# Kernel optimization log

Hardware: AMD Instinct MI355X
Metric: run time of the kernel (lower is better)

Reference implementation:

```python
import jax, jax.numpy as jnp
import numpy as np

B, T, N = 8, 12, 400
C0, C1, C2 = 64, 64, 128
KS, KT, H = 3, 3, 4  # Cheb order (KS+1 kernels), temporal kernel, heads
DN = ('NHWC', 'HWIO', 'NHWC')


def setup_inputs() -> dict:
    key = jax.random.key(0)
    ks = jax.random.split(key, 12)
    rn = lambda k, shp, s: jax.random.normal(k, shp, jnp.float32) * s
    inputs = jax.random.normal(ks[0], (B, T, N, C0), jnp.float32)
    supports = rn(ks[1], (KS + 1, N, N), 0.05)           # dense Cheb poly kernels
    adj_mask = (jax.random.uniform(ks[2], (N, N)) < 0.05) | jnp.eye(N, dtype=bool)
    wt1 = rn(ks[3], (KT, 1, C0, 2 * C1), 0.1)            # GLU temporal conv
    bt1 = jnp.zeros((2 * C1,), jnp.float32)
    Wf = rn(ks[4], (H, C1, C1), 0.1)                     # per-head feature proj
    a_src = rn(ks[5], (H, C1), 0.1)
    a_dst = rn(ks[6], (H, C1), 0.1)
    Wcheb = rn(ks[7], (H, KS + 1, C1, C1), 0.1)          # per-head per-hop weights
    wt2 = rn(ks[8], (KT, 1, C1, C2), 0.1)                # relu temporal conv
    bt2 = jnp.zeros((C2,), jnp.float32)
    gamma = jnp.ones((1, 1, N, C2), jnp.float32)
    beta = jnp.zeros((1, 1, N, C2), jnp.float32)
    return dict(inputs=inputs, supports=supports, adj_mask=adj_mask, wt1=wt1,
                bt1=bt1, Wf=Wf, a_src=a_src, a_dst=a_dst, Wcheb=Wcheb,
                wt2=wt2, bt2=bt2, gamma=gamma, beta=beta)


def reference(inputs, supports, adj_mask, wt1, bt1, Wf, a_src, a_dst, Wcheb,
              wt2, bt2, gamma, beta):
    # --- temporal conv 1 (GLU), c_in == c_out so residual is the raw input ---
    conv = jax.lax.conv_general_dilated(inputs, wt1, (1, 1), 'VALID',
                                        dimension_numbers=DN) + bt1
    res = inputs[:, KT - 1:]                              # [B, T-Kt+1, N, C1]
    x = (conv[..., :C1] + res) * jax.nn.sigmoid(conv[..., C1:])

    # --- spatial attention-weighted Chebyshev graph conv (batched over B*T') ---
    b, t = x.shape[0], x.shape[1]
    xf = x.reshape(b * t, N, C1)                          # [Bt, N, C1]
    f = jnp.einsum('bnc,hco->bhno', xf, Wf)               # [Bt, H, N, C1]
    e_src = jnp.einsum('bhnc,hc->bhn', f, a_src)
    e_dst = jnp.einsum('bhnc,hc->bhn', f, a_dst)
    logits = jax.nn.leaky_relu(e_src[:, :, :, None] + e_dst[:, :, None, :], 0.2)
    logits = jnp.where(adj_mask, logits, -1e9)            # mask to graph edges
    alpha = jax.nn.softmax(logits, axis=-1)               # [Bt, H, N, N]
    out = jnp.zeros((b * t, H, N, C1), xf.dtype)
    for k in range(KS + 1):                               # small fixed hop loop
        msg = jnp.einsum('bhij,bjc->bhic', alpha * supports[k], xf)
        out = out + jnp.einsum('bhic,hco->bhio', msg, Wcheb[:, k])
    gc = out.mean(axis=1).reshape(x.shape)                # head average (is_concat=False)
    x = jax.nn.relu(gc + x)                               # residual, c_in == c_out

    # --- temporal conv 2 (relu), c_in=C1 < c_out=C2 -> zero-pad residual ---
    conv2 = jax.lax.conv_general_dilated(x, wt2, (1, 1), 'VALID',
                                         dimension_numbers=DN) + bt2
    res2 = jnp.pad(x[:, KT - 1:], ((0, 0), (0, 0), (0, 0), (0, C2 - C1)))
    y = jax.nn.relu(conv2 + res2)                         # [B, T-2(Kt-1), N, C2]

    # --- per-sample-per-step norm over (node, channel), then dropout=0 (identity) ---
    mu = jnp.mean(y, axis=(2, 3), keepdims=True)
    var = jnp.var(y, axis=(2, 3), keepdims=True)
    return (y - mu) / jnp.sqrt(var + 1e-6) * gamma + beta
```

## Files before the change

### kernel.cpp

```cpp
#include <hip/hip_runtime.h>
#include <hip/hip_bf16.h>

#define NB 8
#define NT 12
#define NN 400
#define NC0 64
#define NC1 64
#define NC2 128
#define NH 4
#define NSUP 4
#define NT1 10
#define NT2 8
#define NBT 80
#define NROW 32000
#define NROW2 25600

typedef unsigned short ushort_t;
typedef ushort_t ushort8 __attribute__((ext_vector_type(8)));
typedef ushort_t ushort4v __attribute__((ext_vector_type(4)));
typedef __attribute__((ext_vector_type(8))) short bf16x8;
typedef __attribute__((ext_vector_type(4))) float f32x4;

#define WAVE_SYNC() asm volatile("s_waitcnt lgkmcnt(0)" ::: "memory")

__device__ __forceinline__ float bf2f(ushort_t u) {
    union { unsigned int i; float f; } x; x.i = ((unsigned int)u) << 16; return x.f;
}
__device__ __forceinline__ ushort_t f2bf(float f) {
    union { float f; unsigned int i; } x; x.f = f;
    unsigned int r = x.i + 0x7fff + ((x.i >> 16) & 1);
    return (ushort_t)(r >> 16);
}
__device__ __forceinline__ unsigned cvtpk_bf16(float lo, float hi) {
    unsigned r;
    asm volatile("v_cvt_pk_bf16_f32 %0, %1, %2" : "=v"(r) : "v"(lo), "v"(hi));
    return r;
}

__global__ __launch_bounds__(256) void kprep_all(
    const float* __restrict__ in,
    const float* __restrict__ wt1, const float* __restrict__ wt2, const float* __restrict__ wch,
    const float* __restrict__ Wf, const float* __restrict__ a_src, const float* __restrict__ a_dst,
    const void* __restrict__ adj, const float* __restrict__ supports,
    ushort_t* __restrict__ xbf,
    ushort_t* __restrict__ Bt1f, ushort_t* __restrict__ Bt2f, ushort_t* __restrict__ Btf,
    ushort_t* __restrict__ Bu,
    int* __restrict__ rowcnt, int* __restrict__ rowidx, float* __restrict__ supc) {
    int bid = blockIdx.x;
    if (bid < 2400) {
        int idx = bid * 256 + threadIdx.x;
        const float4* v4 = (const float4*)in;
        float4 v = v4[idx];
        ushort4v o = { f2bf(v.x), f2bf(v.y), f2bf(v.z), f2bf(v.w) };
        *(ushort4v*)(xbf + idx * 4) = o;
    } else if (bid < 2496) {
        int f = (bid - 2400) * 256 + threadIdx.x;
        int i = f & 7, lane = (f >> 3) & 63, grp = f >> 9;
        int kb = grp % 6, q = grp / 6;
        int n = q * 16 + (lane & 15);
        int k = kb * 32 + (lane >> 4) * 8 + i;
        Bt1f[f] = f2bf(wt1[k * 128 + n]);
    } else if (bid < 2592) {
        int f = (bid - 2496) * 256 + threadIdx.x;
        int i = f & 7, lane = (f >> 3) & 63, grp = f >> 9;
        int kb = grp % 6, q = grp / 6;
        int n = q * 16 + (lane & 15);
        int k = kb * 32 + (lane >> 4) * 8 + i;
        Bt2f[f] = f2bf(wt2[k * 128 + n]);
    } else if (bid < 2848) {
        int f = (bid - 2592) * 256 + threadIdx.x;
        int i = f & 7, lane = (f >> 3) & 63;
        int kb = (f >> 9) & 31, nt = f >> 14;
        int n = nt * 16 + (lane & 15);
        int k = kb * 32 + (lane >> 4) * 8 + i;
        Btf[f] = f2bf(wch[k * 64 + n]);
    } else if (bid == 2848) {
        int tid = threadIdx.x;
        int h = tid >> 6, c = tid & 63;
        const float* w = Wf + (h * 64 + c) * 64;
        float s1 = 0.f, s2 = 0.f;
        #pragma unroll 8
        for (int o = 0; o < 64; o++) {
            s1 += w[o] * a_src[h * 64 + o];
            s2 += w[o] * a_dst[h * 64 + o];
        }
        int ks = c >> 5, kq = (c & 31) >> 3, i = c & 7;
        int baseidx = ks * 512 + (kq * 16) * 8 + i;
        Bu[baseidx + (h) * 8]      = f2bf(s1);
        Bu[baseidx + (4 + h) * 8]  = f2bf(s2);
        Bu[baseidx + (8 + h) * 8]  = 0;
        Bu[baseidx + (12 + h) * 8] = 0;
    } else {
        int wid = threadIdx.x >> 6, lane = threadIdx.x & 63;
        int i = (bid - 2849) * 4 + wid;
        if (i >= NN) return;
        int f = ((const unsigned char*)adj)[401] != 0;
        const unsigned char* ab = (const unsigned char*)adj;
        const int* ai = (const int*)adj;
        int cnt = 0;
        for (int base = 0; base < NN; base += 64) {
            int j = base + lane;
            bool m = false;
            if (j < NN) m = f ? (ab[(size_t)i * NN + j] != 0) : (ai[(size_t)i * NN + j] != 0);
            unsigned long long mask = __ballot(m);
            int pre = __popcll(mask & ((1ull << lane) - 1ull));
            if (m) {
                int t = cnt + pre;
                rowidx[i * NN + t] = j;
                if (t < 64) {
                    float4 sv;
                    sv.x = supports[0 * 160000 + i * 400 + j];
                    sv.y = supports[1 * 160000 + i * 400 + j];
                    sv.z = supports[2 * 160000 + i * 400 + j];
                    sv.w = supports[3 * 160000 + i * 400 + j];
                    *(float4*)(supc + ((size_t)i * 64 + t) * 4) = sv;
                }
            }
            cnt += __popcll(mask);
        }
        if (lane >= cnt && lane < 64) {
            float4 z = make_float4(0.f, 0.f, 0.f, 0.f);
            *(float4*)(supc + ((size_t)i * 64 + lane) * 4) = z;
        }
        if (lane == 0) rowcnt[i] = cnt;
    }
}

__global__ __launch_bounds__(256) void k3_conv1(
    const ushort_t* __restrict__ xbf, const float* __restrict__ in,
    const ushort_t* __restrict__ Bt1f, const float* __restrict__ bt1,
    const ushort_t* __restrict__ Bu,
    ushort_t* __restrict__ xb2,
    float* __restrict__ es4, float* __restrict__ ed4) {
    __shared__ ushort_t xs[4][16 * 64];
    int wid = threadIdx.x >> 6, lane = threadIdx.x & 63;
    int m = lane & 15, kq = lane >> 4;
    int r0 = blockIdx.x * 64 + wid * 16;

    int pos = r0 + m; int bt = pos / NN; int n = pos - bt * NN;
    int b = bt / NT1; int t = bt - b * NT1;
    const ushort_t* abase = xbf + ((size_t)((b * NT + t) * NN) + n) * NC0;

    f32x4 acc[8];
    #pragma unroll
    for (int q = 0; q < 8; q++) acc[q] = (f32x4){0.f, 0.f, 0.f, 0.f};

    #pragma unroll
    for (int kb = 0; kb < 6; kb++) {
        int k0 = kb * 32 + kq * 8;
        int kt = k0 >> 6, c = k0 & 63;
        bf16x8 a = *(const bf16x8*)(abase + kt * (NN * NC0) + c);
        #pragma unroll
        for (int q = 0; q < 8; q++) {
            bf16x8 bf = *(const bf16x8*)(Bt1f + (((q * 6 + kb) * 64 + lane) << 3));
            acc[q] = __builtin_amdgcn_mfma_f32_16x16x32_bf16(a, bf, acc[q], 0, 0, 0);
        }
    }

    float b0[4], b1[4];
    #pragma unroll
    for (int q = 0; q < 4; q++) {
        int col = q * 16 + m;
        b0[q] = bt1[col]; b1[q] = bt1[64 + col];
    }

    char* xsw = (char*)&xs[wid][0];
    #pragma unroll
    for (int r = 0; r < 4; r++) {
        int row = 4 * kq + r;
        int pr = r0 + row;
        int btr = pr / NN; int nr = pr - btr * NN;
        int br = btr / NT1; int tr = btr - br * NT1;
        const float* resp = in + ((size_t)((br * NT + tr + 2) * NN) + nr) * NC0;
        int swr = (row & 7) << 4;
        ushort_t xh[4];
        #pragma unroll
        for (int q = 0; q < 4; q++) {
            int col = q * 16 + m;
            float a0 = acc[q][r] + b0[q];
            float a1 = acc[q + 4][r] + b1[q];
            float res = resp[col];
            float g = 1.f / (1.f + __expf(-a1));
            float xv = (a0 + res) * g;
            xh[q] = f2bf(xv);
            *(ushort_t*)(xsw + (row * 128 + ((col * 2) ^ swr))) = xh[q];
        }
        ushort4v o = { xh[0], xh[1], xh[2], xh[3] };
        *(ushort4v*)(xb2 + (size_t)pr * 64 + m * 4) = o;
    }
    WAVE_SYNC();

    f32x4 eacc = (f32x4){0.f, 0.f, 0.f, 0.f};
    int swm = (m & 7) << 4;
    #pragma unroll
    for (int ks = 0; ks < 2; ks++) {
        bf16x8 af = *(const bf16x8*)(xsw + (m * 128 + ((ks * 64 + kq * 16) ^ swm)));
        bf16x8 bu = *(const bf16x8*)(Bu + ks * 512 + (lane << 3));
        eacc = __builtin_amdgcn_mfma_f32_16x16x32_bf16(af, bu, eacc, 0, 0, 0);
    }
    if (m < 8) {
        #pragma unroll
        for (int r = 0; r < 4; r++) {
            int pr = r0 + 4 * kq + r;
            if (m < 4) es4[(size_t)pr * 4 + m] = eacc[r];
            else       ed4[(size_t)pr * 4 + (m - 4)] = eacc[r];
        }
    }
}

__global__ __launch_bounds__(512) void k4_fused(
    const float* __restrict__ es4, const float* __restrict__ ed4,
    const ushort_t* __restrict__ xb2, const float* __restrict__ supc,
    const int* __restrict__ rowcnt, const int* __restrict__ rowidx,
    const ushort_t* __restrict__ Btf, ushort_t* __restrict__ x2b) {
    __shared__ float alpha[8][4][68];
    __shared__ float supv[8][4][68];
    __shared__ int   jidx[8][64];
    __shared__ ushort_t amem[16 * 1024];

    int wv = threadIdx.x >> 6, lane = threadIdx.x & 63;
    int base = blockIdx.x * 16;
    int bt = base / NN;
    int i0 = base - bt * NN;
    const float* edb = ed4 + (size_t)bt * NN * 4;
    const ushort_t* xbB = xb2 + (size_t)bt * NN * NC1;
    int g = lane >> 4;
    int m16 = lane & 15, hA = m16 >> 2, kA = m16 & 3;

    #pragma unroll 1
    for (int p = 0; p < 2; p++) {
        int lr = p * 8 + wv;
        int i = i0 + lr;
        int row = base + lr;
        int deg = rowcnt[i]; if (deg > 64) deg = 64;

        int t = lane;
        bool act = t < deg;
        int j = act ? rowidx[(size_t)i * NN + t] : 0;
        jidx[wv][t] = j;
        float4 esv = *(const float4*)(es4 + (size_t)row * 4);
        float4 e = *(const float4*)(edb + (size_t)j * 4);
        float4 sp = *(const float4*)(supc + ((size_t)i * 64 + t) * 4);
        WAVE_SYNC();

        int4 ja = *(const int4*)&jidx[wv][8 * g];
        int4 jb = *(const int4*)&jidx[wv][8 * g + 4];
        const ushort_t* xg = xbB + m16 * 4;
        uint2 g0 = *(const uint2*)(xg + (size_t)ja.x * 64);
        uint2 g1 = *(const uint2*)(xg + (size_t)ja.y * 64);
        uint2 g2 = *(const uint2*)(xg + (size_t)ja.z * 64);
        uint2 g3 = *(const uint2*)(xg + (size_t)ja.w * 64);
        uint2 g4 = *(const uint2*)(xg + (size_t)jb.x * 64);
        uint2 g5 = *(const uint2*)(xg + (size_t)jb.y * 64);
        uint2 g6 = *(const uint2*)(xg + (size_t)jb.z * 64);
        uint2 g7 = *(const uint2*)(xg + (size_t)jb.w * 64);

        float l0 = esv.x + e.x; l0 = fmaxf(l0, 0.2f * l0);
        float l1 = esv.y + e.y; l1 = fmaxf(l1, 0.2f * l1);
        float l2 = esv.z + e.z; l2 = fmaxf(l2, 0.2f * l2);
        float l3 = esv.w + e.w; l3 = fmaxf(l3, 0.2f * l3);
        float p0 = act ? __expf(l0) : 0.f;
        float p1 = act ? __expf(l1) : 0.f;
        float p2 = act ? __expf(l2) : 0.f;
        float p3 = act ? __expf(l3) : 0.f;
        float s0 = p0, s1 = p1, s2 = p2, s3 = p3;
        #pragma unroll
        for (int off = 32; off >= 1; off >>= 1) {
            s0 += __shfl_xor(s0, off, 64);
            s1 += __shfl_xor(s1, off, 64);
            s2 += __shfl_xor(s2, off, 64);
            s3 += __shfl_xor(s3, off, 64);
        }
        alpha[wv][0][t] = p0 / s0;
        alpha[wv][1][t] = p1 / s1;
        alpha[wv][2][t] = p2 / s2;
        alpha[wv][3][t] = p3 / s3;
        supv[wv][0][t] = sp.x;
        supv[wv][1][t] = sp.y;
        supv[wv][2][t] = sp.z;
        supv[wv][3][t] = sp.w;
        WAVE_SYNC();

        f32x4 acc[4];
        #pragma unroll
        for (int n = 0; n < 4; n++) acc[n] = (f32x4){0.f, 0.f, 0.f, 0.f};

        {
            const float* ap  = &alpha[wv][hA][8 * g];
            const float* spp = &supv[wv][kA][8 * g];
            float4 aa = *(const float4*)ap;
            float4 ab = *(const float4*)(ap + 4);
            float4 sa = *(const float4*)spp;
            float4 sb = *(const float4*)(spp + 4);
            union { unsigned u[4]; bf16x8 v; } af;
            af.u[0] = cvtpk_bf16(aa.x * sa.x, aa.y * sa.y);
            af.u[1] = cvtpk_bf16(aa.z * sa.z, aa.w * sa.w);
            af.u[2] = cvtpk_bf16(ab.x * sb.x, ab.y * sb.y);
            af.u[3] = cvtpk_bf16(ab.z * sb.z, ab.w * sb.w);

            union { unsigned u[4]; bf16x8 v; } b0, b1, b2, b3;
            b0.u[0] = __builtin_amdgcn_perm(g1.x, g0.x, 0x05040100u);
            b1.u[0] = __builtin_amdgcn_perm(g1.x, g0.x, 0x07060302u);
            b2.u[0] = __builtin_amdgcn_perm(g1.y, g0.y, 0x05040100u);
            b3.u[0] = __builtin_amdgcn_perm(g1.y, g0.y, 0x07060302u);
            b0.u[1] = __builtin_amdgcn_perm(g3.x, g2.x, 0x05040100u);
            b1.u[1] = __builtin_amdgcn_perm(g3.x, g2.x, 0x07060302u);
            b2.u[1] = __builtin_amdgcn_perm(g3.y, g2.y, 0x05040100u);
            b3.u[1] = __builtin_amdgcn_perm(g3.y, g2.y, 0x07060302u);
            b0.u[2] = __builtin_amdgcn_perm(g5.x, g4.x, 0x05040100u);
            b1.u[2] = __builtin_amdgcn_perm(g5.x, g4.x, 0x07060302u);
            b2.u[2] = __builtin_amdgcn_perm(g5.y, g4.y, 0x05040100u);
            b3.u[2] = __builtin_amdgcn_perm(g5.y, g4.y, 0x07060302u);
            b0.u[3] = __builtin_amdgcn_perm(g7.x, g6.x, 0x05040100u);
            b1.u[3] = __builtin_amdgcn_perm(g7.x, g6.x, 0x07060302u);
            b2.u[3] = __builtin_amdgcn_perm(g7.y, g6.y, 0x05040100u);
            b3.u[3] = __builtin_amdgcn_perm(g7.y, g6.y, 0x07060302u);

            acc[0] = __builtin_amdgcn_mfma_f32_16x16x32_bf16(af.v, b0.v, acc[0], 0, 0, 0);
            acc[1] = __builtin_amdgcn_mfma_f32_16x16x32_bf16(af.v, b1.v, acc[1], 0, 0, 0);
            acc[2] = __builtin_amdgcn_mfma_f32_16x16x32_bf16(af.v, b2.v, acc[2], 0, 0, 0);
            acc[3] = __builtin_amdgcn_mfma_f32_16x16x32_bf16(af.v, b3.v, acc[3], 0, 0, 0);
        }

        if (deg > 32) {
            int4 ja2 = *(const int4*)&jidx[wv][32 + 8 * g];
            int4 jb2 = *(const int4*)&jidx[wv][32 + 8 * g + 4];
            uint2 h0 = *(const uint2*)(xg + (size_t)ja2.x * 64);
            uint2 h1 = *(const uint2*)(xg + (size_t)ja2.y * 64);
            uint2 h2 = *(const uint2*)(xg + (size_t)ja2.z * 64);
            uint2 h3 = *(const uint2*)(xg + (size_t)ja2.w * 64);
            uint2 h4 = *(const uint2*)(xg + (size_t)jb2.x * 64);
            uint2 h5 = *(const uint2*)(xg + (size_t)jb2.y * 64);
            uint2 h6 = *(const uint2*)(xg + (size_t)jb2.z * 64);
            uint2 h7 = *(const uint2*)(xg + (size_t)jb2.w * 64);
            const float* ap  = &alpha[wv][hA][32 + 8 * g];
            const float* spp = &supv[wv][kA][32 + 8 * g];
            float4 aa = *(const float4*)ap;
            float4 ab = *(const float4*)(ap + 4);
            float4 sa = *(const float4*)spp;
            float4 sb = *(const float4*)(spp + 4);
            union { unsigned u[4]; bf16x8 v; } af;
            af.u[0] = cvtpk_bf16(aa.x * sa.x, aa.y * sa.y);
            af.u[1] = cvtpk_bf16(aa.z * sa.z, aa.w * sa.w);
            af.u[2] = cvtpk_bf16(ab.x * sb.x, ab.y * sb.y);
            af.u[3] = cvtpk_bf16(ab.z * sb.z, ab.w * sb.w);
            union { unsigned u[4]; bf16x8 v; } b0, b1, b2, b3;
            b0.u[0] = __builtin_amdgcn_perm(h1.x, h0.x, 0x05040100u);
            b1.u[0] = __builtin_amdgcn_perm(h1.x, h0.x, 0x07060302u);
            b2.u[0] = __builtin_amdgcn_perm(h1.y, h0.y, 0x05040100u);
            b3.u[0] = __builtin_amdgcn_perm(h1.y, h0.y, 0x07060302u);
            b0.u[1] = __builtin_amdgcn_perm(h3.x, h2.x, 0x05040100u);
            b1.u[1] = __builtin_amdgcn_perm(h3.x, h2.x, 0x07060302u);
            b2.u[1] = __builtin_amdgcn_perm(h3.y, h2.y, 0x05040100u);
            b3.u[1] = __builtin_amdgcn_perm(h3.y, h2.y, 0x07060302u);
            b0.u[2] = __builtin_amdgcn_perm(h5.x, h4.x, 0x05040100u);
            b1.u[2] = __builtin_amdgcn_perm(h5.x, h4.x, 0x07060302u);
            b2.u[2] = __builtin_amdgcn_perm(h5.y, h4.y, 0x05040100u);
            b3.u[2] = __builtin_amdgcn_perm(h5.y, h4.y, 0x07060302u);
            b0.u[3] = __builtin_amdgcn_perm(h7.x, h6.x, 0x05040100u);
            b1.u[3] = __builtin_amdgcn_perm(h7.x, h6.x, 0x07060302u);
            b2.u[3] = __builtin_amdgcn_perm(h7.y, h6.y, 0x05040100u);
            b3.u[3] = __builtin_amdgcn_perm(h7.y, h6.y, 0x07060302u);
            acc[0] = __builtin_amdgcn_mfma_f32_16x16x32_bf16(af.v, b0.v, acc[0], 0, 0, 0);
            acc[1] = __builtin_amdgcn_mfma_f32_16x16x32_bf16(af.v, b1.v, acc[1], 0, 0, 0);
            acc[2] = __builtin_amdgcn_mfma_f32_16x16x32_bf16(af.v, b2.v, acc[2], 0, 0, 0);
            acc[3] = __builtin_amdgcn_mfma_f32_16x16x32_bf16(af.v, b3.v, acc[3], 0, 0, 0);
        }

        char* arow = (char*)amem + lr * 2048;
        int swl = (lr & 7) << 4;
        #pragma unroll
        for (int n = 0; n < 4; n++) {
            #pragma unroll
            for (int r2 = 0; r2 < 2; r2++) {
                union { unsigned u; ushort_t h[2]; } pk;
                pk.u = cvtpk_bf16(acc[n][2 * r2], acc[n][2 * r2 + 1]);
                int tb = ((4 * g + 2 * r2) * 64 + n * 16 + m16) * 2;
                *(ushort_t*)(arow + (tb ^ swl)) = pk.h[0];
                *(ushort_t*)(arow + ((tb + 128) ^ swl)) = pk.h[1];
            }
        }
        WAVE_SYNC();
    }
    __syncthreads();

    f32x4 acc0 = (f32x4){0.f, 0.f, 0.f, 0.f};
    f32x4 acc1 = (f32x4){0.f, 0.f, 0.f, 0.f};
    int kq = g;
    int nt = wv & 3, kh = wv >> 2;
    const ushort_t* bfr = Btf + (((size_t)(nt * 32 + kh * 16)) << 9) + (lane << 3);
    const char* abase = (const char*)amem + m16 * 2048;
    int swm = (m16 & 7) << 4;

    #pragma unroll
    for (int kbl = 0; kbl < 16; kbl += 2) {
        int kb = kh * 16 + kbl;
        bf16x8 a0 = *(const bf16x8*)(abase + ((kb * 64 + kq * 16) ^ swm));
        bf16x8 b0 = *(const bf16x8*)(bfr + (kbl << 9));
        acc0 = __builtin_amdgcn_mfma_f32_16x16x32_bf16(a0, b0, acc0, 0, 0, 0);
        bf16x8 a1 = *(const bf16x8*)(abase + (((kb + 1) * 64 + kq * 16) ^ swm));
        bf16x8 b1 = *(const bf16x8*)(bfr + ((kbl + 1) << 9));
        acc1 = __builtin_amdgcn_mfma_f32_16x16x32_bf16(a1, b1, acc1, 0, 0, 0);
    }
    f32x4 s = acc0 + acc1;

    f32x4* redv = (f32x4*)alpha;
    if (kh == 1) redv[nt * 64 + lane] = s;
    __syncthreads();
    if (kh == 0) {
        f32x4 o = redv[nt * 64 + lane];
        s.x += o.x; s.y += o.y; s.z += o.z; s.w += o.w;
        #pragma unroll
        for (int r = 0; r < 4; r++) {
            int grow = base + kq * 4 + r;
            int col = nt * 16 + m16;
            float xres = bf2f(xb2[(size_t)grow * 64 + m16 * 4 + nt]);
            float v = fmaxf(0.f, 0.25f * s[r] + xres);
            x2b[(size_t)grow * 64 + col] = f2bf(v);
        }
    }
}

__global__ __launch_bounds__(256) void k6_conv2(
    const ushort_t* __restrict__ x2b,
    const ushort_t* __restrict__ Bt2f, const float* __restrict__ bt2,
    float* __restrict__ out, float* __restrict__ part2) {
    int wid = threadIdx.x >> 6, lane = threadIdx.x & 63;
    int m = lane & 15, kq = lane >> 4;
    int r0 = blockIdx.x * 64 + wid * 16;
    int blkbase = blockIdx.x * 64;
    int btp0 = blkbase / 400;
    int lim = (btp0 + 1) * 400;

    int pos = r0 + m; int btp = pos / NN; int n = pos - btp * NN;
    int b = btp >> 3; int t2 = btp & 7;
    const ushort_t* abase = x2b + ((size_t)((b * NT1 + t2) * NN) + n) * NC1;

    f32x4 acc[8];
    #pragma unroll
    for (int q = 0; q < 8; q++) acc[q] = (f32x4){0.f, 0.f, 0.f, 0.f};

    #pragma unroll
    for (int kb = 0; kb < 6; kb++) {
        int k0 = kb * 32 + kq * 8;
        int kt = k0 >> 6, c = k0 & 63;
        bf16x8 a = *(const bf16x8*)(abase + kt * (NN * NC1) + c);
        #pragma unroll
        for (int q = 0; q < 8; q++) {
            bf16x8 bf = *(const bf16x8*)(Bt2f + (((q * 6 + kb) * 64 + lane) << 3));
            acc[q] = __builtin_amdgcn_mfma_f32_16x16x32_bf16(a, bf, acc[q], 0, 0, 0);
        }
    }

    float sA1 = 0.f, sA2 = 0.f, sB1 = 0.f, sB2 = 0.f;
    #pragma unroll
    for (int r = 0; r < 4; r++) {
        int pr = r0 + 4 * kq + r;
        int btr = pr / NN; int nr = pr - btr * NN;
        int br = btr >> 3; int tr = btr & 7;
        const ushort_t* resp = x2b + ((size_t)((br * NT1 + tr + 2) * NN) + nr) * NC1;
        bool inA = pr < lim;
        #pragma unroll
        for (int q = 0; q < 8; q++) {
            int col = q * 16 + m;
            float v = acc[q][r] + bt2[col];
            if (q < 4) v += bf2f(resp[col]);
            v = fmaxf(v, 0.f);
            out[(size_t)pr * NC2 + col] = v;
            if (inA) { sA1 += v; sA2 = fmaf(v, v, sA2); }
            else     { sB1 += v; sB2 = fmaf(v, v, sB2); }
        }
    }
    #pragma unroll
    for (int off = 32; off >= 1; off >>= 1) {
        sA1 += __shfl_xor(sA1, off, 64);
        sA2 += __shfl_xor(sA2, off, 64);
        sB1 += __shfl_xor(sB1, off, 64);
        sB2 += __shfl_xor(sB2, off, 64);
    }
    __shared__ float red[4][4];
    if (lane == 0) { red[wid][0] = sA1; red[wid][1] = sA2; red[wid][2] = sB1; red[wid][3] = sB2; }
    __syncthreads();
    if (threadIdx.x < 4) {
        float v = red[0][threadIdx.x] + red[1][threadIdx.x] + red[2][threadIdx.x] + red[3][threadIdx.x];
        part2[blockIdx.x * 4 + threadIdx.x] = v;
    }
}

__global__ __launch_bounds__(256) void k7b(float* __restrict__ y, const float* __restrict__ part2,
                                           const float* __restrict__ gamma, const float* __restrict__ beta) {
    int g = blockIdx.x >> 3, sl = blockIdx.x & 7;
    int b0 = (g * 400) >> 6;
    int b1 = (g * 400 + 399) >> 6;
    float S1 = 0.f, S2 = 0.f;
    for (int b = b0; b <= b1; b++) {
        int bg = (b * 64) / 400;
        if (bg == g)     { S1 += part2[b * 4];     S2 += part2[b * 4 + 1]; }
        if (bg + 1 == g) { S1 += part2[b * 4 + 2]; S2 += part2[b * 4 + 3]; }
    }
    const float invM = 1.f / 51200.f;
    float mu = S1 * invM;
    float var = S2 * invM - mu * mu;
    float rs = rsqrtf(var + 1e-6f);
    float4* p = (float4*)(y + (size_t)g * 51200 + sl * 6400);
    const float4* gp = (const float4*)(gamma + sl * 6400);
    const float4* bp = (const float4*)(beta + sl * 6400);
    for (int idx = threadIdx.x; idx < 1600; idx += 256) {
        float4 v = p[idx];
        float4 g4 = gp[idx];
        float4 b4 = bp[idx];
        v.x = (v.x - mu) * rs * g4.x + b4.x;
        v.y = (v.y - mu) * rs * g4.y + b4.y;
        v.z = (v.z - mu) * rs * g4.z + b4.z;
        v.w = (v.w - mu) * rs * g4.w + b4.w;
        p[idx] = v;
    }
}

extern "C" void kernel_launch(void* const* d_in, const int* in_sizes, int n_in,
                              void* d_out, int out_size, void* d_ws, size_t ws_size,
                              hipStream_t stream) {
    const float* inputs   = (const float*)d_in[0];
    const float* supports = (const float*)d_in[1];
    const void*  adj      = d_in[2];
    const float* wt1      = (const float*)d_in[3];
    const float* bt1      = (const float*)d_in[4];
    const float* Wf       = (const float*)d_in[5];
    const float* a_src    = (const float*)d_in[6];
    const float* a_dst    = (const float*)d_in[7];
    const float* Wcheb    = (const float*)d_in[8];
    const float* wt2      = (const float*)d_in[9];
    const float* bt2      = (const float*)d_in[10];
    const float* gamma    = (const float*)d_in[11];
    const float* beta     = (const float*)d_in[12];

    char* ws = (char*)d_ws;
    const size_t OES   = 0;
    const size_t OED   = OES   + 512000;
    const size_t OBU   = OED   + 512000;
    const size_t OCNT  = OBU   + 2048;
    const size_t OIDX  = OCNT  + 2048;
    const size_t OBT   = OIDX  + 640000;
    const size_t OBT1  = OBT   + 131072;
    const size_t OBT2  = OBT1  + 49152;
    const size_t OXBF  = OBT2  + 49152;
    const size_t OX2B  = OXBF  + 4915200;
    const size_t OXB   = OX2B  + 4096000;
    const size_t OSUP  = OXB   + 4096000;
    const size_t OPRT  = OSUP  + 409600;
    const size_t NEED  = OPRT  + 8192;
    if (ws_size < NEED) return;

    float* es4    = (float*)(ws + OES);
    float* ed4    = (float*)(ws + OED);
    ushort_t* Bu  = (ushort_t*)(ws + OBU);
    int*   rowcnt = (int*)(ws + OCNT);
    int*   rowidx = (int*)(ws + OIDX);
    ushort_t* Btf = (ushort_t*)(ws + OBT);
    ushort_t* Bt1f= (ushort_t*)(ws + OBT1);
    ushort_t* Bt2f= (ushort_t*)(ws + OBT2);
    ushort_t* xbf = (ushort_t*)(ws + OXBF);
    ushort_t* x2b = (ushort_t*)(ws + OX2B);
    ushort_t* xb2 = (ushort_t*)(ws + OXB);
    float* supc   = (float*)(ws + OSUP);
    float* part2  = (float*)(ws + OPRT);
    float* out    = (float*)d_out;

    hipLaunchKernelGGL(kprep_all, dim3(2949), dim3(256), 0, stream,
                       inputs, wt1, wt2, Wcheb, Wf, a_src, a_dst, adj, supports,
                       xbf, Bt1f, Bt2f, Btf, Bu, rowcnt, rowidx, supc);
    hipLaunchKernelGGL(k3_conv1, dim3(NROW / 64), dim3(256), 0, stream,
                       xbf, inputs, Bt1f, bt1, Bu, xb2, es4, ed4);
    hipLaunchKernelGGL(k4_fused, dim3(NROW / 16), dim3(512), 0, stream,
                       es4, ed4, xb2, supc, rowcnt, rowidx, Btf, x2b);
    hipLaunchKernelGGL(k6_conv2, dim3(NROW2 / 64), dim3(256), 0, stream, x2b, Bt2f, bt2, out, part2);
    hipLaunchKernelGGL(k7b, dim3(512), dim3(256), 0, stream, out, part2, gamma, beta);
}
```

Measured before the change: 72.37 us.

## Fuse layer norm into conv2 via grid-wide atomic barrier

Removes the separate normalization kernel. conv2 now keeps its relu outputs in registers, publishes per-block partial sums, and waits at a software grid barrier built on an atomic counter. Each block then reads the group statistics and writes the normalized output directly, which saves one launch and a full read-modify-write of the output. The barrier depends on all 400 blocks being resident at the same time, and the spin-wait plus the atomics add latency.

```diff
diff --git a/kernel.cpp b/kernel.cpp
--- a/kernel.cpp
+++ b/kernel.cpp
@@ -45,7 +45,8 @@
     ushort_t* __restrict__ xbf,
     ushort_t* __restrict__ Bt1f, ushort_t* __restrict__ Bt2f, ushort_t* __restrict__ Btf,
     ushort_t* __restrict__ Bu,
-    int* __restrict__ rowcnt, int* __restrict__ rowidx, float* __restrict__ supc) {
+    int* __restrict__ rowcnt, int* __restrict__ rowidx, float* __restrict__ supc,
+    int* __restrict__ cnt) {
     int bid = blockIdx.x;
     if (bid < 2400) {
         int idx = bid * 256 + threadIdx.x;
@@ -76,6 +77,7 @@
         Btf[f] = f2bf(wch[k * 64 + n]);
     } else if (bid == 2848) {
         int tid = threadIdx.x;
+        if (tid == 0) *cnt = 0;
         int h = tid >> 6, c = tid & 63;
         const float* w = Wf + (h * 64 + c) * 64;
         float s1 = 0.f, s2 = 0.f;
@@ -97,7 +99,7 @@
         int f = ((const unsigned char*)adj)[401] != 0;
         const unsigned char* ab = (const unsigned char*)adj;
         const int* ai = (const int*)adj;
-        int cnt = 0;
+        int cnt2 = 0;
         for (int base = 0; base < NN; base += 64) {
             int j = base + lane;
             bool m = false;
@@ -105,7 +107,7 @@
             unsigned long long mask = __ballot(m);
             int pre = __popcll(mask & ((1ull << lane) - 1ull));
             if (m) {
-                int t = cnt + pre;
+                int t = cnt2 + pre;
                 rowidx[i * NN + t] = j;
                 if (t < 64) {
                     float4 sv;
@@ -116,13 +118,13 @@
                     *(float4*)(supc + ((size_t)i * 64 + t) * 4) = sv;
                 }
             }
-            cnt += __popcll(mask);
-        }
-        if (lane >= cnt && lane < 64) {
+            cnt2 += __popcll(mask);
+        }
+        if (lane >= cnt2 && lane < 64) {
             float4 z = make_float4(0.f, 0.f, 0.f, 0.f);
             *(float4*)(supc + ((size_t)i * 64 + lane) * 4) = z;
         }
-        if (lane == 0) rowcnt[i] = cnt;
+        if (lane == 0) rowcnt[i] = cnt2;
     }
 }
 
@@ -424,13 +426,15 @@
 __global__ __launch_bounds__(256) void k6_conv2(
     const ushort_t* __restrict__ x2b,
     const ushort_t* __restrict__ Bt2f, const float* __restrict__ bt2,
-    float* __restrict__ out, float* __restrict__ part2) {
+    const float* __restrict__ gamma, const float* __restrict__ beta,
+    float* __restrict__ out, float* __restrict__ part2, int* __restrict__ cnt) {
     int wid = threadIdx.x >> 6, lane = threadIdx.x & 63;
     int m = lane & 15, kq = lane >> 4;
     int r0 = blockIdx.x * 64 + wid * 16;
     int blkbase = blockIdx.x * 64;
-    int btp0 = blkbase / 400;
-    int lim = (btp0 + 1) * 400;
+    int gA = blkbase / 400;
+    int gB = (blkbase + 63) / 400;
+    int lim = (gA + 1) * 400;
 
     int pos = r0 + m; int btp = pos / NN; int n = pos - btp * NN;
     int b = btp >> 3; int t2 = btp & 7;
@@ -466,7 +470,7 @@
             float v = acc[q][r] + bt2[col];
             if (q < 4) v += bf2f(resp[col]);
             v = fmaxf(v, 0.f);
-            out[(size_t)pr * NC2 + col] = v;
+            acc[q][r] = v;
             if (inA) { sA1 += v; sA2 = fmaf(v, v, sA2); }
             else     { sB1 += v; sB2 = fmaf(v, v, sB2); }
         }
@@ -483,37 +487,57 @@
     __syncthreads();
     if (threadIdx.x < 4) {
         float v = red[0][threadIdx.x] + red[1][threadIdx.x] + red[2][threadIdx.x] + red[3][threadIdx.x];
-        part2[blockIdx.x * 4 + threadIdx.x] = v;
-    }
-}
-
-__global__ __launch_bounds__(256) void k7b(float* __restrict__ y, const float* __restrict__ part2,
-                                           const float* __restrict__ gamma, const float* __restrict__ beta) {
-    int g = blockIdx.x >> 3, sl = blockIdx.x & 7;
-    int b0 = (g * 400) >> 6;
-    int b1 = (g * 400 + 399) >> 6;
-    float S1 = 0.f, S2 = 0.f;
-    for (int b = b0; b <= b1; b++) {
-        int bg = (b * 64) / 400;
-        if (bg == g)     { S1 += part2[b * 4];     S2 += part2[b * 4 + 1]; }
-        if (bg + 1 == g) { S1 += part2[b * 4 + 2]; S2 += part2[b * 4 + 3]; }
+        __hip_atomic_store(&part2[blockIdx.x * 4 + threadIdx.x], v,
+                           __ATOMIC_RELEASE, __HIP_MEMORY_SCOPE_AGENT);
+    }
+    __syncthreads();
+    if (threadIdx.x == 0) {
+        __hip_atomic_fetch_add(cnt, 1, __ATOMIC_ACQ_REL, __HIP_MEMORY_SCOPE_AGENT);
+        while (__hip_atomic_load(cnt, __ATOMIC_ACQUIRE, __HIP_MEMORY_SCOPE_AGENT) < 400) {}
+    }
+    __syncthreads();
+
+    float S1A = 0.f, S2A = 0.f, S1B = 0.f, S2B = 0.f;
+    {
+        int b0 = (gA * 400) >> 6, b1 = (gA * 400 + 399) >> 6;
+        for (int bb = b0; bb <= b1; bb++) {
+            int bg = (bb * 64) / 400;
+            if (bg == gA)     { S1A += __hip_atomic_load(&part2[bb * 4],     __ATOMIC_RELAXED, __HIP_MEMORY_SCOPE_AGENT);
+                                S2A += __hip_atomic_load(&part2[bb * 4 + 1], __ATOMIC_RELAXED, __HIP_MEMORY_SCOPE_AGENT); }
+            if (bg + 1 == gA) { S1A += __hip_atomic_load(&part2[bb * 4 + 2], __ATOMIC_RELAXED, __HIP_MEMORY_SCOPE_AGENT);
+                                S2A += __hip_atomic_load(&part2[bb * 4 + 3], __ATOMIC_RELAXED, __HIP_MEMORY_SCOPE_AGENT); }
+        }
+    }
+    if (gB != gA) {
+        int b0 = (gB * 400) >> 6, b1 = (gB * 400 + 399) >> 6;
+        for (int bb = b0; bb <= b1; bb++) {
+            int bg = (bb * 64) / 400;
+            if (bg == gB)     { S1B += __hip_atomic_load(&part2[bb * 4],     __ATOMIC_RELAXED, __HIP_MEMORY_SCOPE_AGENT);
+                                S2B += __hip_atomic_load(&part2[bb * 4 + 1], __ATOMIC_RELAXED, __HIP_MEMORY_SCOPE_AGENT); }
+            if (bg + 1 == gB) { S1B += __hip_atomic_load(&part2[bb * 4 + 2], __ATOMIC_RELAXED, __HIP_MEMORY_SCOPE_AGENT);
+                                S2B += __hip_atomic_load(&part2[bb * 4 + 3], __ATOMIC_RELAXED, __HIP_MEMORY_SCOPE_AGENT); }
+        }
     }
     const float invM = 1.f / 51200.f;
-    float mu = S1 * invM;
-    float var = S2 * invM - mu * mu;
-    float rs = rsqrtf(var + 1e-6f);
-    float4* p = (float4*)(y + (size_t)g * 51200 + sl * 6400);
-    const float4* gp = (const float4*)(gamma + sl * 6400);
-    const float4* bp = (const float4*)(beta + sl * 6400);
-    for (int idx = threadIdx.x; idx < 1600; idx += 256) {
-        float4 v = p[idx];
-        float4 g4 = gp[idx];
-        float4 b4 = bp[idx];
-        v.x = (v.x - mu) * rs * g4.x + b4.x;
-        v.y = (v.y - mu) * rs * g4.y + b4.y;
-        v.z = (v.z - mu) * rs * g4.z + b4.z;
-        v.w = (v.w - mu) * rs * g4.w + b4.w;
-        p[idx] = v;
+    float muA = S1A * invM;
+    float rsA = rsqrtf(S2A * invM - muA * muA + 1e-6f);
+    float muB = S1B * invM;
+    float rsB = rsqrtf(S2B * invM - muB * muB + 1e-6f);
+
+    #pragma unroll
+    for (int r = 0; r < 4; r++) {
+        int pr = r0 + 4 * kq + r;
+        bool inA = pr < lim;
+        float mu = inA ? muA : muB;
+        float rs = inA ? rsA : rsB;
+        int gg = inA ? gA : gB;
+        int nr = pr - gg * 400;
+        #pragma unroll
+        for (int q = 0; q < 8; q++) {
+            int col = q * 16 + m;
+            float v = acc[q][r];
+            out[(size_t)pr * NC2 + col] = (v - mu) * rs * gamma[nr * NC2 + col] + beta[nr * NC2 + col];
+        }
     }
 }
 
@@ -548,7 +572,8 @@
     const size_t OXB   = OX2B  + 4096000;
     const size_t OSUP  = OXB   + 4096000;
     const size_t OPRT  = OSUP  + 409600;
-    const size_t NEED  = OPRT  + 8192;
+    const size_t OBAR  = OPRT  + 8192;
+    const size_t NEED  = OBAR  + 256;
     if (ws_size < NEED) return;
 
     float* es4    = (float*)(ws + OES);
@@ -564,15 +589,16 @@
     ushort_t* xb2 = (ushort_t*)(ws + OXB);
     float* supc   = (float*)(ws + OSUP);
     float* part2  = (float*)(ws + OPRT);
+    int*   cnt    = (int*)(ws + OBAR);
     float* out    = (float*)d_out;
 
     hipLaunchKernelGGL(kprep_all, dim3(2949), dim3(256), 0, stream,
                        inputs, wt1, wt2, Wcheb, Wf, a_src, a_dst, adj, supports,
-                       xbf, Bt1f, Bt2f, Btf, Bu, rowcnt, rowidx, supc);
+                       xbf, Bt1f, Bt2f, Btf, Bu, rowcnt, rowidx, supc, cnt);
     hipLaunchKernelGGL(k3_conv1, dim3(NROW / 64), dim3(256), 0, stream,
                        xbf, inputs, Bt1f, bt1, Bu, xb2, es4, ed4);
     hipLaunchKernelGGL(k4_fused, dim3(NROW / 16), dim3(512), 0, stream,
                        es4, ed4, xb2, supc, rowcnt, rowidx, Btf, x2b);
-    hipLaunchKernelGGL(k6_conv2, dim3(NROW2 / 64), dim3(256), 0, stream, x2b, Bt2f, bt2, out, part2);
-    hipLaunchKernelGGL(k7b, dim3(512), dim3(256), 0, stream, out, part2, gamma, beta);
-}
+    hipLaunchKernelGGL(k6_conv2, dim3(NROW2 / 64), dim3(256), 0, stream,
+                       x2b, Bt2f, bt2, gamma, beta, out, part2, cnt);
+}
```

Result: slower. 94.97 us (+31.2%).
